# Optimization experiments

Hardware: AMD Instinct MI355X
Metric: run time of the kernel (lower is better)

## Reference

```python
import jax, jax.numpy as jnp
import numpy as np

KNOWLEDGE_RANK = 128
COARSE_K = 20
FINE_K = 10


def setup_inputs() -> dict:
    key = jax.random.key(0)
    ks = jax.random.split(key, 5)
    B, S, D, N, R = 2, 2048, 1024, 65536, KNOWLEDGE_RANK
    return {
        "x": jax.random.normal(ks[0], (B, S, D), dtype=jnp.float32),
        "W_router": jax.random.normal(ks[1], (D, N), dtype=jnp.float32) * (1.0 / np.sqrt(D)),
        "W_enc": jax.random.normal(ks[2], (D, R), dtype=jnp.float32) * (1.0 / np.sqrt(D)),
        "K_all": jax.random.normal(ks[3], (N, R), dtype=jnp.float32) * 0.02,
        "V_all": jax.random.normal(ks[4], (N, D), dtype=jnp.float32) * 0.02,
    }


def reference(x, W_router, W_enc, K_all, V_all):
    # x: [B,S,D]; router logits over the knowledge table: [B,S,N]
    k_logits = jnp.einsum('bsd,dn->bsn', x, W_router)
    coarse_scores, candidate_idx = jax.lax.top_k(k_logits, COARSE_K)  # [B,S,C]

    query = jnp.einsum('bsd,dr->bsr', x, W_enc)  # [B,S,R]
    K_cand = K_all[candidate_idx]                # [B,S,C,R] irregular gather
    fine_scores = jnp.einsum('bsr,bscr->bsc', query, K_cand) / np.sqrt(KNOWLEDGE_RANK)

    fine_topk_scores, fine_local_idx = jax.lax.top_k(fine_scores, FINE_K)  # [B,S,F]
    fine_weights = jax.nn.softmax(fine_topk_scores, axis=-1)               # [B,S,F]
    fine_global_idx = jnp.take_along_axis(candidate_idx, fine_local_idx, axis=-1)  # [B,S,F]

    selected_V = V_all[fine_global_idx]          # [B,S,F,D] irregular gather
    output = jnp.einsum('bsfd,bsf->bsd', selected_V, fine_weights)
    return output
```

## Files before the change

### kernel.cpp

```cpp
#include <hip/hip_runtime.h>
#include <math.h>
#include <stdint.h>

#define NTOK 4096
#define DIM  1024
#define NCOL 65536
#define RANK 128
#define CK 20
#define FK 10

#define SLABS 16
#define SLABCOLS (NCOL / SLABS)
#define BM 128
#define BN 256
#define BK 32
#define NCHUNK (SLABCOLS / BN)
#define KSTEPS (DIM / BK)
#define CKS 12
#define NPART (SLABS * CKS)
#define POOL 32
#define SELSTRIDE 132

typedef _Float16 f16;
typedef __attribute__((ext_vector_type(8))) _Float16 f16x8;
typedef __attribute__((ext_vector_type(4))) float f32x4;

__device__ __forceinline__ void f32_split(float v, unsigned short& h, unsigned short& l) {
    f16 hh = (f16)v;
    float r = v - (float)hh;
    f16 ll = (f16)r;
    h = __builtin_bit_cast(unsigned short, hh);
    l = __builtin_bit_cast(unsigned short, ll);
}

__device__ __forceinline__ void gll16(const void* src, void* ldsdst) {
    __builtin_amdgcn_global_load_lds(
        (__attribute__((address_space(1))) unsigned int*)src,
        (__attribute__((address_space(3))) unsigned int*)ldsdst, 16, 0, 0);
}

#define WAITVM_(n) asm volatile("s_waitcnt vmcnt(" #n ")" ::: "memory")
#define WAITLGKM0  asm volatile("s_waitcnt lgkmcnt(0)" ::: "memory")

__global__ __launch_bounds__(256)
void k0_convx(const float* __restrict__ x, unsigned short* __restrict__ xh)
{
    int i = blockIdx.x * 256 + threadIdx.x;
    float4 v = ((const float4*)x)[i];
    ushort4 h; unsigned short dummy;
    f32_split(v.x, h.x, dummy); f32_split(v.y, h.y, dummy);
    f32_split(v.z, h.z, dummy); f32_split(v.w, h.w, dummy);
    ((ushort4*)xh)[i] = h;
}

__global__ __launch_bounds__(256)
void k0_convw(const float* __restrict__ W, unsigned short* __restrict__ WhT,
              unsigned short* __restrict__ WlT)
{
    __shared__ float t[64][65];
    const int tid = threadIdx.x;
    const int k0 = blockIdx.x * 64;
    const int n0 = blockIdx.y * 64;
#pragma unroll
    for (int i = 0; i < 16; ++i) {
        int idx = i * 256 + tid;
        int r = idx >> 6, c = idx & 63;
        t[r][c] = W[(size_t)(k0 + r) * NCOL + n0 + c];
    }
    __syncthreads();
#pragma unroll
    for (int i = 0; i < 8; ++i) {
        int idx = i * 256 + tid;
        int n = idx >> 5, kp = idx & 31;
        float a = t[2 * kp][n]     * 1024.0f;
        float b = t[2 * kp + 1][n] * 1024.0f;
        unsigned short ah, al, bh, bl;
        f32_split(a, ah, al);
        f32_split(b, bh, bl);
        unsigned int wh = (unsigned)ah | ((unsigned)bh << 16);
        unsigned int wl = (unsigned)al | ((unsigned)bl << 16);
        size_t row = (size_t)(n0 + n) * DIM + k0;
        *(unsigned int*)(WhT + row + 2 * kp) = wh;
        *(unsigned int*)(WlT + row + 2 * kp) = wl;
    }
}

__global__ __launch_bounds__(256)
void k_query(const float* __restrict__ x, const float* __restrict__ Wenc,
             float* __restrict__ Q)
{
    const int tid  = threadIdx.x;
    const int r    = tid & 127;
    const int tg   = tid >> 7;
    const int tok0 = blockIdx.x * 8 + tg * 4;
    const float* x0 = x + (size_t)tok0 * DIM;
    float a0 = 0.f, a1 = 0.f, a2 = 0.f, a3 = 0.f;
#pragma unroll 8
    for (int d = 0; d < DIM; ++d) {
        float w = Wenc[(size_t)d * RANK + r];
        a0 = fmaf(x0[d],            w, a0);
        a1 = fmaf(x0[DIM + d],      w, a1);
        a2 = fmaf(x0[2 * DIM + d],  w, a2);
        a3 = fmaf(x0[3 * DIM + d],  w, a3);
    }
    Q[(size_t)(tok0 + 0) * RANK + r] = a0;
    Q[(size_t)(tok0 + 1) * RANK + r] = a1;
    Q[(size_t)(tok0 + 2) * RANK + r] = a2;
    Q[(size_t)(tok0 + 3) * RANK + r] = a3;
}

__global__ __launch_bounds__(512, 4)
void k1_mfma(const unsigned short* __restrict__ xh,
             const unsigned short* __restrict__ WhT,
             float* __restrict__ part_s, int* __restrict__ part_i)
{
    __shared__ __align__(16) unsigned char smem[73728];

    const int tid  = threadIdx.x;
    const int lane = tid & 63;
    const int wave = tid >> 6;
    const int wr = wave >> 2;
    const int wc = wave & 3;
    const int slab = blockIdx.x;
    const int tokbase = blockIdx.y * BM;

    const int srow = tid >> 2;
    const int soct = (tid & 3) ^ ((tid >> 3) & 3);
    const unsigned short* pA = xh + (size_t)(tokbase + srow) * DIM + soct * 8;

    const int c4 = lane & 15;
    const int xj = (((lane >> 4) ^ ((c4 >> 1) & 3)) << 4);
    const int offA0 =        (wr * 64 + c4) * 64 + xj;
    const int offB0 = 8192 + (wc * 64 + c4) * 64 + xj;

    float ts[CKS]; int ti[CKS];
#pragma unroll
    for (int k = 0; k < CKS; ++k) { ts[k] = -INFINITY; ti[k] = 0x7fffffff; }

    float* sel = (float*)smem;

    #define STAGE(pb, buf, kk) do {                                              \
        unsigned b_ = (unsigned)(buf) * 24576u + (unsigned)wave * 1024u;         \
        gll16(pA   + (size_t)(kk) * BK,                smem + b_);               \
        gll16((pb) + (size_t)(kk) * BK,                smem + b_ + 8192);        \
        gll16((pb) + (size_t)128 * DIM + (kk) * BK,    smem + b_ + 16384);       \
    } while (0)

    #define INS1(v_, ci_) do {                                                    \
        if ((v_) > ts[CKS - 1]) {                                                 \
            float cv = (v_); int ci = (ci_);                                      \
            _Pragma("unroll")                                                     \
            for (int k = 0; k < CKS; ++k) {                                       \
                bool g = cv > ts[k];                                              \
                float os = ts[k]; int oi = ti[k];                                 \
                ts[k] = g ? cv : os; ti[k] = g ? ci : oi;                         \
                cv = g ? os : cv;   ci = g ? oi : ci;                             \
            }                                                                     \
        }                                                                         \
    } while (0)

#pragma unroll 1
    for (int nc = 0; nc < NCHUNK; ++nc) {
        const int n0 = slab * SLABCOLS + nc * BN;
        const unsigned short* pB = WhT + (size_t)(n0 + srow) * DIM + soct * 8;

        f32x4 acc[4][4];
        const f32x4 zero = {0.f, 0.f, 0.f, 0.f};
#pragma unroll
        for (int m = 0; m < 4; ++m)
#pragma unroll
            for (int n = 0; n < 4; ++n) acc[m][n] = zero;

        STAGE(pB, 0, 0);
        STAGE(pB, 1, 1);

#pragma unroll 1
        for (int kk = 0; kk < KSTEPS; ++kk) {
            if (kk + 1 < KSTEPS) {
                WAITVM_(3);
            } else {
                WAITVM_(0);
            }
            __builtin_amdgcn_s_barrier();

            if (kk + 2 < KSTEPS)
                STAGE(pB, (kk + 2) % 3, kk + 2);

            const unsigned char* bp = smem + (unsigned)(kk % 3) * 24576u;
            f16x8 Af[4];
#pragma unroll
            for (int m = 0; m < 4; ++m) Af[m] = *(const f16x8*)(bp + offA0 + m * 1024);
#pragma unroll
            for (int n = 0; n < 4; ++n) {
                f16x8 Bf = *(const f16x8*)(bp + offB0 + n * 1024);
#pragma unroll
                for (int m = 0; m < 4; ++m)
                    acc[m][n] = __builtin_amdgcn_mfma_f32_16x16x32_f16(Af[m], Bf, acc[m][n], 0, 0, 0);
            }

            WAITLGKM0;
        }
        __builtin_amdgcn_s_barrier();

#pragma unroll 1
        for (int p = 0; p < 2; ++p) {
            if ((wc >> 1) == p) {
                const int colb = (wc & 1) * 64;
#pragma unroll
                for (int m = 0; m < 4; ++m)
#pragma unroll
                    for (int n = 0; n < 4; ++n) {
                        const int col = colb + n * 16 + c4;
                        const int row = wr * 64 + m * 16 + (lane >> 4) * 4;
#pragma unroll
                        for (int r = 0; r < 4; ++r)
                            sel[(row + r) * SELSTRIDE + col] = acc[m][n][r];
                    }
            }
            __syncthreads();
            {
                const int part = tid & 3;
                const float* rp = sel + (tid >> 2) * SELSTRIDE + part;
                const int ibase = n0 + p * 128 + part;
#pragma unroll 1
                for (int j = 0; j < 32; ++j) {
                    float v = rp[4 * j];
                    INS1(v, ibase + 4 * j);
                }
            }
            __syncthreads();
        }
    }
    #undef STAGE

    float* Ls = (float*)smem;
    int*   Li = (int*)(smem + 24576);
#pragma unroll
    for (int k = 0; k < CKS; ++k) {
        Ls[tid * CKS + k] = ts[k];
        Li[tid * CKS + k] = ti[k];
    }
    __syncthreads();
    if (tid < BM) {
        const int b0 = (tid * 4 + 0) * CKS, b1 = (tid * 4 + 1) * CKS;
        const int b2 = (tid * 4 + 2) * CKS, b3 = (tid * 4 + 3) * CKS;
        int h0 = 0, h1 = 0, h2 = 0, h3 = 0;
        const size_t ob = ((size_t)(tokbase + tid) * SLABS + slab) * CKS;
#pragma unroll 1
        for (int k = 0; k < CKS; ++k) {
            float s0 = Ls[b0 + h0]; int i0 = Li[b0 + h0];
            float s1 = Ls[b1 + h1]; int i1 = Li[b1 + h1];
            float s2 = Ls[b2 + h2]; int i2 = Li[b2 + h2];
            float s3 = Ls[b3 + h3]; int i3 = Li[b3 + h3];
            float bs = s0; int bi = i0; int bp = 0;
            if (s1 > bs || (s1 == bs && i1 < bi)) { bs = s1; bi = i1; bp = 1; }
            if (s2 > bs || (s2 == bs && i2 < bi)) { bs = s2; bi = i2; bp = 2; }
            if (s3 > bs || (s3 == bs && i3 < bi)) { bs = s3; bi = i3; bp = 3; }
            part_s[ob + k] = bs; part_i[ob + k] = bi;
            if      (bp == 0) ++h0;
            else if (bp == 1) ++h1;
            else if (bp == 2) ++h2;
            else              ++h3;
        }
    }
}

__global__ __launch_bounds__(256)
void k3_fine(const float* __restrict__ x, const float* __restrict__ Q,
             const float* __restrict__ Kall, const float* __restrict__ Vall,
             const unsigned short* __restrict__ WhT, const unsigned short* __restrict__ WlT,
             const float* __restrict__ part_s, const int* __restrict__ part_i,
             float* __restrict__ out)
{
    const int tok = blockIdx.x;
    const int tid = threadIdx.x;

    __shared__ float xs[DIM];
    __shared__ float qs[RANK];
    __shared__ float ls[NPART];
    __shared__ int   li[NPART];
    __shared__ int   pool[POOL];
    __shared__ float resc[POOL];
    __shared__ int   cand[CK];
    __shared__ float fsc[CK];
    __shared__ float fss[FK];
    __shared__ int   fgi[FK];
    __shared__ float fw[FK];

    ((float4*)xs)[tid] = ((const float4*)(x + (size_t)tok * DIM))[tid];
    if (tid < NPART) {
        ls[tid] = part_s[(size_t)tok * NPART + tid];
        li[tid] = part_i[(size_t)tok * NPART + tid];
    }
    if (tid < RANK) qs[tid] = Q[(size_t)tok * RANK + tid];
    __syncthreads();

    if (tid < NPART) {
        float s = ls[tid]; int idx = li[tid];
        int r = 0;
        for (int e = 0; e < NPART; ++e) {
            float s2 = ls[e]; int i2 = li[e];
            r += (s2 > s) || (s2 == s && i2 < idx);
        }
        if (r < POOL) pool[r] = idx;
    }
    __syncthreads();

    {
        const int c = tid >> 3, oct = tid & 7;
        const int idx = pool[c];
        const ushort4* ph = (const ushort4*)(WhT + (size_t)idx * DIM + oct * 128);
        const ushort4* pl = (const ushort4*)(WlT + (size_t)idx * DIM + oct * 128);
        const float* xp = xs + oct * 128;
        float a = 0.0f;
#pragma unroll 4
        for (int j = 0; j < 32; ++j) {
            ushort4 hv = ph[j], lv = pl[j];
            a = fmaf(xp[j*4+0], (float)__builtin_bit_cast(f16, hv.x) + (float)__builtin_bit_cast(f16, lv.x), a);
            a = fmaf(xp[j*4+1], (float)__builtin_bit_cast(f16, hv.y) + (float)__builtin_bit_cast(f16, lv.y), a);
            a = fmaf(xp[j*4+2], (float)__builtin_bit_cast(f16, hv.z) + (float)__builtin_bit_cast(f16, lv.z), a);
            a = fmaf(xp[j*4+3], (float)__builtin_bit_cast(f16, hv.w) + (float)__builtin_bit_cast(f16, lv.w), a);
        }
        a += __shfl_down(a, 4, 8);
        a += __shfl_down(a, 2, 8);
        a += __shfl_down(a, 1, 8);
        if (oct == 0) resc[c] = a * (1.0f / 1024.0f);
    }
    __syncthreads();

    if (tid < POOL) {
        float s = resc[tid]; int idx = pool[tid];
        int r = 0;
        for (int e = 0; e < POOL; ++e)
            r += (resc[e] > s) || (resc[e] == s && pool[e] < idx);
        if (r < CK) cand[r] = idx;
    }
    __syncthreads();

    if (tid < CK) {
        const float* Kr = Kall + (size_t)cand[tid] * RANK;
        float s = 0.0f;
#pragma unroll 8
        for (int r = 0; r < RANK; ++r) s = fmaf(qs[r], Kr[r], s);
        fsc[tid] = s * 0.08838834764831845f;
    }
    __syncthreads();

    if (tid < CK) {
        float s = fsc[tid]; int r = 0;
        for (int e = 0; e < CK; ++e)
            r += (fsc[e] > s) || (fsc[e] == s && e < tid);
        if (r < FK) { fss[r] = s; fgi[r] = cand[tid]; }
    }
    __syncthreads();

    if (tid == 0) {
        float m = fss[0];
#pragma unroll
        for (int k = 1; k < FK; ++k) m = fmaxf(m, fss[k]);
        float w[FK]; float sum = 0.0f;
#pragma unroll
        for (int k = 0; k < FK; ++k) { w[k] = expf(fss[k] - m); sum += w[k]; }
        float inv = 1.0f / sum;
#pragma unroll
        for (int k = 0; k < FK; ++k) fw[k] = w[k] * inv;
    }
    __syncthreads();

#pragma unroll
    for (int jj = 0; jj < DIM / 256; ++jj) {
        const int d = tid + jj * 256;
        float o = 0.0f;
#pragma unroll
        for (int f = 0; f < FK; ++f)
            o = fmaf(fw[f], Vall[(size_t)fgi[f] * DIM + d], o);
        out[(size_t)tok * DIM + d] = o;
    }
}

__global__ __launch_bounds__(256, 2)
void k1_router_f32(const float* __restrict__ x, const float* __restrict__ Wr,
                   float* __restrict__ part_s, int* __restrict__ part_i)
{
    __shared__ float smem[64][257];
    const int tid     = threadIdx.x;
    const int tokbase = blockIdx.x * 64;
    const int colbase = blockIdx.y * 8192;
    const int mytok   = tid & 63;
    const int mypart  = tid >> 6;

    float ts[CK]; int ti[CK];
#pragma unroll
    for (int k = 0; k < CK; ++k) { ts[k] = -INFINITY; ti[k] = 0x7fffffff; }

#pragma unroll 1
    for (int cg = 0; cg < 32; ++cg) {
        const int n = colbase + cg * 256 + tid;
        float acc[64];
#pragma unroll
        for (int t = 0; t < 64; ++t) acc[t] = 0.0f;
#pragma unroll 1
        for (int dc = 0; dc < DIM; dc += 8) {
            float w[8];
#pragma unroll
            for (int i = 0; i < 8; ++i)
                w[i] = Wr[(size_t)(dc + i) * NCOL + n];
#pragma unroll
            for (int t = 0; t < 64; ++t) {
                const float* xr = x + (size_t)(tokbase + t) * DIM + dc;
#pragma unroll
                for (int i = 0; i < 8; ++i)
                    acc[t] = fmaf(xr[i], w[i], acc[t]);
            }
        }
        __syncthreads();
#pragma unroll
        for (int t = 0; t < 64; ++t) smem[t][tid] = acc[t];
        __syncthreads();
        const int jbase = mypart * 64;
#pragma unroll 1
        for (int j = 0; j < 64; ++j) {
            float v = smem[mytok][jbase + j];
            if (v > ts[CK - 1]) {
                float cv = v; int ci = colbase + cg * 256 + jbase + j;
#pragma unroll
                for (int k = 0; k < CK; ++k) {
                    bool g = cv > ts[k];
                    float os = ts[k]; int oi = ti[k];
                    ts[k] = g ? cv : os; ti[k] = g ? ci : oi;
                    cv = g ? os : cv;   ci = g ? oi : ci;
                }
            }
        }
    }
    __syncthreads();
    float* Ls = &smem[0][0];
    int*   Li = (int*)(Ls + 256 * CK);
#pragma unroll
    for (int k = 0; k < CK; ++k) { Ls[tid * CK + k] = ts[k]; Li[tid * CK + k] = ti[k]; }
    __syncthreads();
    if (tid < 64) {
        const int tok = tid;
        int h0 = 0, h1 = 0, h2 = 0, h3 = 0;
        const size_t ob = ((size_t)(tokbase + tok) * 8 + blockIdx.y) * CK;
#pragma unroll 1
        for (int k = 0; k < CK; ++k) {
            float s0 = Ls[(      tok) * CK + h0]; int i0 = Li[(      tok) * CK + h0];
            float s1 = Ls[( 64 + tok) * CK + h1]; int i1 = Li[( 64 + tok) * CK + h1];
            float s2 = Ls[(128 + tok) * CK + h2]; int i2 = Li[(128 + tok) * CK + h2];
            float s3 = Ls[(192 + tok) * CK + h3]; int i3 = Li[(192 + tok) * CK + h3];
            float bs = s0; int bi = i0; int bp = 0;
            if (s1 > bs || (s1 == bs && i1 < bi)) { bs = s1; bi = i1; bp = 1; }
            if (s2 > bs || (s2 == bs && i2 < bi)) { bs = s2; bi = i2; bp = 2; }
            if (s3 > bs || (s3 == bs && i3 < bi)) { bs = s3; bi = i3; bp = 3; }
            part_s[ob + k] = bs; part_i[ob + k] = bi;
            if      (bp == 0) ++h0;
            else if (bp == 1) ++h1;
            else if (bp == 2) ++h2;
            else              ++h3;
        }
    }
}

template<int CT, int BLK>
__global__ __launch_bounds__(BLK)
void k3_fine_direct(const float* __restrict__ x, const float* __restrict__ Wenc,
                    const float* __restrict__ Kall, const float* __restrict__ Vall,
                    const float* __restrict__ part_s, const int* __restrict__ part_i,
                    float* __restrict__ out)
{
    const int tok = blockIdx.x;
    const int tid = threadIdx.x;

    __shared__ float xs[DIM];
    __shared__ float qs[RANK];
    __shared__ float ls[CT * CK];
    __shared__ int   li[CT * CK];
    __shared__ int   cand[CK];
    __shared__ float fsc[CK];
    __shared__ float fss[FK];
    __shared__ int   fgi[FK];
    __shared__ float fw[FK];

    if (tid < DIM / 4)
        ((float4*)xs)[tid] = ((const float4*)(x + (size_t)tok * DIM))[tid];
    for (int i = tid; i < CT * CK; i += BLK) {
        ls[i] = part_s[(size_t)tok * (CT * CK) + i];
        li[i] = part_i[(size_t)tok * (CT * CK) + i];
    }
    __syncthreads();

    if (tid < CT * CK) {
        float s = ls[tid]; int idx = li[tid];
        int r = 0;
        for (int e = 0; e < CT * CK; ++e) {
            float s2 = ls[e]; int i2 = li[e];
            r += (s2 > s) || (s2 == s && i2 < idx);
        }
        if (r < CK) cand[r] = idx;
    }
    __syncthreads();

    if (tid < RANK) {
        float q = 0.0f;
#pragma unroll 8
        for (int d = 0; d < DIM; ++d)
            q = fmaf(xs[d], Wenc[(size_t)d * RANK + tid], q);
        qs[tid] = q;
    }
    __syncthreads();

    if (tid < CK) {
        const float* Kr = Kall + (size_t)cand[tid] * RANK;
        float s = 0.0f;
#pragma unroll 8
        for (int r = 0; r < RANK; ++r) s = fmaf(qs[r], Kr[r], s);
        fsc[tid] = s * 0.08838834764831845f;
    }
    __syncthreads();

    if (tid < CK) {
        float s = fsc[tid]; int r = 0;
        for (int e = 0; e < CK; ++e)
            r += (fsc[e] > s) || (fsc[e] == s && e < tid);
        if (r < FK) { fss[r] = s; fgi[r] = cand[tid]; }
    }
    __syncthreads();

    if (tid == 0) {
        float m = fss[0];
#pragma unroll
        for (int k = 1; k < FK; ++k) m = fmaxf(m, fss[k]);
        float w[FK]; float sum = 0.0f;
#pragma unroll
        for (int k = 0; k < FK; ++k) { w[k] = expf(fss[k] - m); sum += w[k]; }
        float inv = 1.0f / sum;
#pragma unroll
        for (int k = 0; k < FK; ++k) fw[k] = w[k] * inv;
    }
    __syncthreads();

    for (int d = tid; d < DIM; d += BLK) {
        float o = 0.0f;
#pragma unroll
        for (int f = 0; f < FK; ++f)
            o = fmaf(fw[f], Vall[(size_t)fgi[f] * DIM + d], o);
        out[(size_t)tok * DIM + d] = o;
    }
}

extern "C" void kernel_launch(void* const* d_in, const int* in_sizes, int n_in,
                              void* d_out, int out_size, void* d_ws, size_t ws_size,
                              hipStream_t stream)
{
    (void)in_sizes; (void)n_in; (void)out_size;
    const float* x    = (const float*)d_in[0];
    const float* Wr   = (const float*)d_in[1];
    const float* Wenc = (const float*)d_in[2];
    const float* Kall = (const float*)d_in[3];
    const float* Vall = (const float*)d_in[4];
    float* out = (float*)d_out;

    const size_t off_ps = 0;
    const size_t off_pi = off_ps + (size_t)NTOK * NPART * 4;
    const size_t off_xh = off_pi + (size_t)NTOK * NPART * 4;
    const size_t off_wh = off_xh + (size_t)NTOK * DIM * 2;
    const size_t off_wl = off_wh + (size_t)NCOL * DIM * 2;
    const size_t off_q  = off_wl + (size_t)NCOL * DIM * 2;
    const size_t REQ    = off_q  + (size_t)NTOK * RANK * 4;

    if (ws_size >= REQ) {
        float* part_s = (float*)((char*)d_ws + off_ps);
        int*   part_i = (int*)((char*)d_ws + off_pi);
        unsigned short* xh  = (unsigned short*)((char*)d_ws + off_xh);
        unsigned short* WhT = (unsigned short*)((char*)d_ws + off_wh);
        unsigned short* WlT = (unsigned short*)((char*)d_ws + off_wl);
        float* Q = (float*)((char*)d_ws + off_q);

        k0_convx<<<NTOK * DIM / 1024, 256, 0, stream>>>(x, xh);
        k_query<<<NTOK / 8, 256, 0, stream>>>(x, Wenc, Q);
        k0_convw<<<dim3(DIM / 64, NCOL / 64), 256, 0, stream>>>(Wr, WhT, WlT);
        k1_mfma<<<dim3(SLABS, NTOK / BM), 512, 0, stream>>>(xh, WhT, part_s, part_i);
        k3_fine<<<NTOK, 256, 0, stream>>>(x, Q, Kall, Vall, WhT, WlT, part_s, part_i, out);
    } else {
        float* part_s = (float*)d_ws;
        int*   part_i = (int*)d_ws + (size_t)NTOK * 8 * CK;
        k1_router_f32<<<dim3(NTOK / 64, 8), 256, 0, stream>>>(x, Wr, part_s, part_i);
        k3_fine_direct<8, 256><<<NTOK, 256, 0, stream>>>(x, Wenc, Kall, Vall, part_s, part_i, out);
    }
}
```

Before: 1.261 ms.

## Shrink router GEMM tile to 128x128 with 256-thread blocks and more slabs

The router MFMA kernel moves from 512-thread blocks with a 128x256 tile to 256-thread blocks with a 128x128 tile, and the column dimension is split into 32 slabs instead of 16. Staging, LDS layout, the selection scratch stride and the per-token partial merge are adjusted to match. This is meant to raise occupancy and grid size, since smaller LDS use and smaller blocks let more blocks reside per CU. In exchange, each A tile is reloaded twice as often and there are twice as many partial candidates (384 per token), which the fine kernel's quadratic rank pass must now process with a strided loop.

```diff
diff --git a/kernel.cpp b/kernel.cpp
--- a/kernel.cpp
+++ b/kernel.cpp
@@ -9,17 +9,17 @@
 #define CK 20
 #define FK 10
 
-#define SLABS 16
+#define SLABS 32
 #define SLABCOLS (NCOL / SLABS)
 #define BM 128
-#define BN 256
+#define BN 128
 #define BK 32
 #define NCHUNK (SLABCOLS / BN)
 #define KSTEPS (DIM / BK)
 #define CKS 12
 #define NPART (SLABS * CKS)
 #define POOL 32
-#define SELSTRIDE 132
+#define SELSTRIDE 65
 
 typedef _Float16 f16;
 typedef __attribute__((ext_vector_type(8))) _Float16 f16x8;
@@ -109,18 +109,18 @@
     Q[(size_t)(tok0 + 3) * RANK + r] = a3;
 }
 
-__global__ __launch_bounds__(512, 4)
+__global__ __launch_bounds__(256, 4)
 void k1_mfma(const unsigned short* __restrict__ xh,
              const unsigned short* __restrict__ WhT,
              float* __restrict__ part_s, int* __restrict__ part_i)
 {
-    __shared__ __align__(16) unsigned char smem[73728];
+    __shared__ __align__(16) unsigned char smem[49152];
 
     const int tid  = threadIdx.x;
     const int lane = tid & 63;
     const int wave = tid >> 6;
-    const int wr = wave >> 2;
-    const int wc = wave & 3;
+    const int wr = wave >> 1;
+    const int wc = wave & 1;
     const int slab = blockIdx.x;
     const int tokbase = blockIdx.y * BM;
 
@@ -140,10 +140,11 @@
     float* sel = (float*)smem;
 
     #define STAGE(pb, buf, kk) do {                                              \
-        unsigned b_ = (unsigned)(buf) * 24576u + (unsigned)wave * 1024u;         \
-        gll16(pA   + (size_t)(kk) * BK,                smem + b_);               \
-        gll16((pb) + (size_t)(kk) * BK,                smem + b_ + 8192);        \
-        gll16((pb) + (size_t)128 * DIM + (kk) * BK,    smem + b_ + 16384);       \
+        unsigned b_ = (unsigned)(buf) * 16384u;                                  \
+        gll16(pA   + (size_t)(kk) * BK,                smem + b_ + tid * 16);    \
+        gll16(pA   + (size_t)64 * DIM + (kk) * BK,     smem + b_ + tid * 16 + 4096); \
+        gll16((pb) + (size_t)(kk) * BK,                smem + b_ + 8192 + tid * 16); \
+        gll16((pb) + (size_t)64 * DIM + (kk) * BK,     smem + b_ + 8192 + tid * 16 + 4096); \
     } while (0)
 
     #define INS1(v_, ci_) do {                                                    \
@@ -177,7 +178,7 @@
 #pragma unroll 1
         for (int kk = 0; kk < KSTEPS; ++kk) {
             if (kk + 1 < KSTEPS) {
-                WAITVM_(3);
+                WAITVM_(4);
             } else {
                 WAITVM_(0);
             }
@@ -186,7 +187,7 @@
             if (kk + 2 < KSTEPS)
                 STAGE(pB, (kk + 2) % 3, kk + 2);
 
-            const unsigned char* bp = smem + (unsigned)(kk % 3) * 24576u;
+            const unsigned char* bp = smem + (unsigned)(kk % 3) * 16384u;
             f16x8 Af[4];
 #pragma unroll
             for (int m = 0; m < 4; ++m) Af[m] = *(const f16x8*)(bp + offA0 + m * 1024);
@@ -204,13 +205,12 @@
 
 #pragma unroll 1
         for (int p = 0; p < 2; ++p) {
-            if ((wc >> 1) == p) {
-                const int colb = (wc & 1) * 64;
+            if (wc == p) {
 #pragma unroll
                 for (int m = 0; m < 4; ++m)
 #pragma unroll
                     for (int n = 0; n < 4; ++n) {
-                        const int col = colb + n * 16 + c4;
+                        const int col = n * 16 + c4;
                         const int row = wr * 64 + m * 16 + (lane >> 4) * 4;
 #pragma unroll
                         for (int r = 0; r < 4; ++r)
@@ -219,13 +219,13 @@
             }
             __syncthreads();
             {
-                const int part = tid & 3;
-                const float* rp = sel + (tid >> 2) * SELSTRIDE + part;
-                const int ibase = n0 + p * 128 + part;
+                const int part = tid & 1;
+                const float* rp = sel + (tid >> 1) * SELSTRIDE + part;
+                const int ibase = n0 + p * 64 + part;
 #pragma unroll 1
                 for (int j = 0; j < 32; ++j) {
-                    float v = rp[4 * j];
-                    INS1(v, ibase + 4 * j);
+                    float v = rp[2 * j];
+                    INS1(v, ibase + 2 * j);
                 }
             }
             __syncthreads();
@@ -234,7 +234,7 @@
     #undef STAGE
 
     float* Ls = (float*)smem;
-    int*   Li = (int*)(smem + 24576);
+    int*   Li = (int*)(smem + 12288);
 #pragma unroll
     for (int k = 0; k < CKS; ++k) {
         Ls[tid * CKS + k] = ts[k];
@@ -242,25 +242,17 @@
     }
     __syncthreads();
     if (tid < BM) {
-        const int b0 = (tid * 4 + 0) * CKS, b1 = (tid * 4 + 1) * CKS;
-        const int b2 = (tid * 4 + 2) * CKS, b3 = (tid * 4 + 3) * CKS;
-        int h0 = 0, h1 = 0, h2 = 0, h3 = 0;
+        const int b0 = (2 * tid) * CKS, b1 = (2 * tid + 1) * CKS;
+        int h0 = 0, h1 = 0;
         const size_t ob = ((size_t)(tokbase + tid) * SLABS + slab) * CKS;
 #pragma unroll 1
         for (int k = 0; k < CKS; ++k) {
             float s0 = Ls[b0 + h0]; int i0 = Li[b0 + h0];
             float s1 = Ls[b1 + h1]; int i1 = Li[b1 + h1];
-            float s2 = Ls[b2 + h2]; int i2 = Li[b2 + h2];
-            float s3 = Ls[b3 + h3]; int i3 = Li[b3 + h3];
-            float bs = s0; int bi = i0; int bp = 0;
-            if (s1 > bs || (s1 == bs && i1 < bi)) { bs = s1; bi = i1; bp = 1; }
-            if (s2 > bs || (s2 == bs && i2 < bi)) { bs = s2; bi = i2; bp = 2; }
-            if (s3 > bs || (s3 == bs && i3 < bi)) { bs = s3; bi = i3; bp = 3; }
-            part_s[ob + k] = bs; part_i[ob + k] = bi;
-            if      (bp == 0) ++h0;
-            else if (bp == 1) ++h1;
-            else if (bp == 2) ++h2;
-            else              ++h3;
+            bool t1 = (s1 > s0) || (s1 == s0 && i1 < i0);
+            part_s[ob + k] = t1 ? s1 : s0;
+            part_i[ob + k] = t1 ? i1 : i0;
+            if (t1) ++h1; else ++h0;
         }
     }
 }
@@ -288,18 +280,18 @@
     __shared__ float fw[FK];
 
     ((float4*)xs)[tid] = ((const float4*)(x + (size_t)tok * DIM))[tid];
-    if (tid < NPART) {
-        ls[tid] = part_s[(size_t)tok * NPART + tid];
-        li[tid] = part_i[(size_t)tok * NPART + tid];
+    for (int i = tid; i < NPART; i += 256) {
+        ls[i] = part_s[(size_t)tok * NPART + i];
+        li[i] = part_i[(size_t)tok * NPART + i];
     }
     if (tid < RANK) qs[tid] = Q[(size_t)tok * RANK + tid];
     __syncthreads();
 
-    if (tid < NPART) {
-        float s = ls[tid]; int idx = li[tid];
+    for (int e = tid; e < NPART; e += 256) {
+        float s = ls[e]; int idx = li[e];
         int r = 0;
-        for (int e = 0; e < NPART; ++e) {
-            float s2 = ls[e]; int i2 = li[e];
+        for (int e2 = 0; e2 < NPART; ++e2) {
+            float s2 = ls[e2]; int i2 = li[e2];
             r += (s2 > s) || (s2 == s && i2 < idx);
         }
         if (r < POOL) pool[r] = idx;
@@ -580,7 +572,7 @@
         k0_convx<<<NTOK * DIM / 1024, 256, 0, stream>>>(x, xh);
         k_query<<<NTOK / 8, 256, 0, stream>>>(x, Wenc, Q);
         k0_convw<<<dim3(DIM / 64, NCOL / 64), 256, 0, stream>>>(Wr, WhT, WlT);
-        k1_mfma<<<dim3(SLABS, NTOK / BM), 512, 0, stream>>>(xh, WhT, part_s, part_i);
+        k1_mfma<<<dim3(SLABS, NTOK / BM), 256, 0, stream>>>(xh, WhT, part_s, part_i);
         k3_fine<<<NTOK, 256, 0, stream>>>(x, Q, Kall, Vall, WhT, WlT, part_s, part_i, out);
     } else {
         float* part_s = (float*)d_ws;
```

Result: slower. 1.419 ms (+12.5%).
